# Optimization experiments

Measured on AMD Instinct MI355X. Metric: run time of the kernel, lower is better.

## Reference

```python
import jax, jax.numpy as jnp
import numpy as np

N = 50000      # nodes
E = 800000     # edges (before self loops)
DIN = 128      # input_dim
H = 128        # hidden_dim
DOUT = 64      # output_dim
G = 64         # graphs in batch
EATTR = 16     # edge_attr dim (unused by math, kept for signature fidelity)


def _conv_params(key, din, h, scale=0.05):
    ks = jax.random.split(key, 6)
    return dict(
        lin_w=jax.random.normal(ks[0], (din, h), dtype=jnp.float32) * scale,
        lin_b=jnp.zeros((h,), jnp.float32),
        w1=jax.random.normal(ks[1], (2 * h, h), dtype=jnp.float32) * scale,
        b1=jnp.zeros((h,), jnp.float32),
        w2=jax.random.normal(ks[2], (h, h), dtype=jnp.float32) * scale,
        b2=jnp.zeros((h,), jnp.float32),
    )


def setup_inputs() -> dict:
    key = jax.random.key(0)
    ks = jax.random.split(key, 10)
    inp = {
        'x': jax.random.normal(ks[0], (N, DIN), dtype=jnp.float32),
        'edge_index': jax.random.randint(ks[1], (2, E), 0, N),
        'edge_attr': jax.random.normal(ks[2], (E, EATTR), dtype=jnp.float32),
        'batch': jnp.sort(jax.random.randint(ks[3], (N,), 0, G)),
    }
    p1 = _conv_params(ks[4], DIN, H)
    p2 = _conv_params(ks[5], H, H)
    p3 = _conv_params(ks[6], H, H)
    for i, p in enumerate((p1, p2, p3), start=1):
        for k, v in p.items():
            inp[f'c{i}_{k}'] = v
    inp['out_w'] = jax.random.normal(ks[7], (H, DOUT), dtype=jnp.float32) * 0.05
    inp['out_b'] = jnp.zeros((DOUT,), jnp.float32)
    return inp


def mpnn_conv(x, src, dst, lin_w, lin_b, w1, b1, w2, b2):
    # x: [N, din] -> h: [N, H]
    n = x.shape[0]
    h = x @ lin_w + lin_b
    loop = jnp.arange(n)
    s = jnp.concatenate([src, loop])   # x_j (source) indices, self loops appended
    d = jnp.concatenate([dst, loop])   # x_i (target) indices
    z = jnp.concatenate([h[d], h[s]], axis=-1)          # [E+N, 2H]  (cat[x_i, x_j])
    m = jax.nn.relu(z @ w1 + b1) @ w2 + b2              # [E+N, H]
    return jax.ops.segment_sum(m, d, num_segments=n)    # aggr='add' at targets


def reference(x, edge_index, edge_attr, batch,
              c1_lin_w, c1_lin_b, c1_w1, c1_b1, c1_w2, c1_b2,
              c2_lin_w, c2_lin_b, c2_w1, c2_b1, c2_w2, c2_b2,
              c3_lin_w, c3_lin_b, c3_w1, c3_b1, c3_w2, c3_b2,
              out_w, out_b):
    src, dst = edge_index[0], edge_index[1]
    h = jax.nn.relu(mpnn_conv(x, src, dst, c1_lin_w, c1_lin_b, c1_w1, c1_b1, c1_w2, c1_b2))
    h = jax.nn.relu(mpnn_conv(h, src, dst, c2_lin_w, c2_lin_b, c2_w1, c2_b1, c2_w2, c2_b2))
    h = jax.nn.relu(mpnn_conv(h, src, dst, c3_lin_w, c3_lin_b, c3_w1, c3_b1, c3_w2, c3_b2))
    # global_mean_pool over graphs
    sums = jax.ops.segment_sum(h, batch, num_segments=G)                       # [G, H]
    cnts = jax.ops.segment_sum(jnp.ones((h.shape[0],), h.dtype), batch, num_segments=G)
    pooled = sums / jnp.maximum(cnts, 1.0)[:, None]
    return pooled @ out_w + out_b
```

## Files before the change

### kernel.cpp

```cpp
#include <hip/hip_runtime.h>
#include <hip/hip_bf16.h>


typedef _Float16 f16_t;
typedef f16_t f16x2 __attribute__((ext_vector_type(2)));
typedef f16_t f16x8 __attribute__((ext_vector_type(8)));
typedef float f32x4 __attribute__((ext_vector_type(4)));
typedef float f32x2v __attribute__((ext_vector_type(2)));
typedef unsigned int u32;
typedef unsigned short u16;
typedef unsigned char u8;

__device__ __forceinline__ float f16lo(u32 v) {
    return (float)__builtin_bit_cast(f16_t, (u16)(v & 0xffff));
}
__device__ __forceinline__ float f16hi(u32 v) {
    return (float)__builtin_bit_cast(f16_t, (u16)(v >> 16));
}
__device__ __forceinline__ u16 f16b(float x) { return __builtin_bit_cast(u16, (f16_t)x); }
__device__ __forceinline__ u32 f16pack(float x, float y) {
    return (u32)f16b(x) | ((u32)f16b(y) << 16);
}

typedef __attribute__((address_space(1))) void gvoid_t;
typedef __attribute__((address_space(3))) void lvoid_t;
__device__ __forceinline__ void glds16(const void* g, void* l) {
    __builtin_amdgcn_global_load_lds((gvoid_t*)g, (lvoid_t*)l, 16, 0, 0);
}

struct PrepArgs {
    const float* x; f16_t* xb; int totalx;
    const int* ei; int E;
    int* hist; int nbk; int NB;
    const float* lin_w[3]; const float* lin_b[3];
    const float* w1[3]; const float* b1[3]; const float* w2[3];
    f16_t* linw16;
    f16_t* w1T;
    f16_t* W2t;
    float* bias256c;
};

__global__ __launch_bounds__(256) void prep_kernel(PrepArgs A, int nConvB) {
    __shared__ union { int hist[512]; u16 T16[128 * 130]; } shm;
    const int b = blockIdx.x, tid = threadIdx.x;
    const int nTr = 9, nLw = 48, nBias = 3;
    if (b < nTr) {
        int layer = b / 3, which = b % 3;
        const float* src; f16_t* dst;
        if (which == 0)      { src = A.w1[layer];          dst = A.w1T + layer * 32768; }
        else if (which == 1) { src = A.w1[layer] + 16384;  dst = A.w1T + layer * 32768 + 16384; }
        else                 { src = A.w2[layer];          dst = A.W2t + layer * 16384; }
#pragma unroll
        for (int it = 0; it < 16; ++it) {
            int idx = it * 1024 + tid * 4;
            int r = idx >> 7, c = idx & 127;
            float4 v = *(const float4*)(src + idx);
            *(u32*)&shm.T16[r * 130 + c] = f16pack(v.x, v.y);
            *(u32*)&shm.T16[r * 130 + c + 2] = f16pack(v.z, v.w);
        }
        __syncthreads();
#pragma unroll
        for (int it = 0; it < 32; ++it) {
            int o = it * 256 + tid;
            int j = o >> 6, c = (o & 63) * 2;
            u32 w = (u32)shm.T16[c * 130 + j] | ((u32)shm.T16[(c + 1) * 130 + j] << 16);
            ((u32*)dst)[o] = w;
        }
        return;
    }
    if (b < nTr + nLw) {
        int i = (b - nTr) * 1024 + tid * 4;
        int layer = i >> 14, off = i & 16383;
        float4 v = *(const float4*)(A.lin_w[layer] + off);
        *(uint2*)(A.linw16 + i) = make_uint2(f16pack(v.x, v.y), f16pack(v.z, v.w));
        return;
    }
    if (b < nTr + nLw + nBias) {
        int layer = b - nTr - nLw;
        int j = tid;
        const float* w1p = A.w1[layer];
        const float* wcol = (j < 128) ? (w1p + j) : (w1p + 16384 + (j - 128));
        const float* lbp = A.lin_b[layer];
        float s = (j < 128) ? A.b1[layer][j] : 0.f;
        for (int c = 0; c < 128; ++c) s += lbp[c] * wcol[c * 128];
        A.bias256c[layer * 256 + j] = s;
        return;
    }
    if (b < nTr + nLw + nBias + A.NB) {
        const int bb = b - nTr - nLw - nBias;
        const int nbk = A.nbk, E = A.E;
        for (int i = tid; i < nbk; i += 256) shm.hist[i] = 0;
        __syncthreads();
        const int chunk = (E + A.NB - 1) / A.NB;
        const int e0 = bb * chunk, e1 = min(E, e0 + chunk);
        for (int e = e0 + tid; e < e1; e += 256) atomicAdd(&shm.hist[A.ei[E + e] >> 7], 1);
        __syncthreads();
        for (int i = tid; i < nbk; i += 256) A.hist[(size_t)bb * nbk + i] = shm.hist[i];
        return;
    }
    int i = ((b - nTr - nLw - nBias - A.NB) * 256 + tid) * 4;
    if (i >= A.totalx) return;
    float4 v = *(const float4*)(A.x + i);
    *(uint2*)(A.xb + i) = make_uint2(f16pack(v.x, v.y), f16pack(v.z, v.w));
}

__global__ __launch_bounds__(256) void hscan_kernel(int* __restrict__ hist,
                                                    int* __restrict__ bcnt, int nbk, int NB) {
    __shared__ int sh[256];
    const int b = blockIdx.x, t = threadIdx.x;
    int run = 0;
    for (int c0 = 0; c0 < NB; c0 += 256) {
        int idx = c0 + t;
        int v = (idx < NB) ? hist[(size_t)idx * nbk + b] : 0;
        sh[t] = v;
        __syncthreads();
#pragma unroll
        for (int o = 1; o < 256; o <<= 1) {
            int u = (t >= o) ? sh[t - o] : 0;
            __syncthreads();
            sh[t] += u;
            __syncthreads();
        }
        if (idx < NB) hist[(size_t)idx * nbk + b] = run + sh[t] - v;
        int tot = sh[255];
        __syncthreads();
        run += tot;
    }
    if (t == 0) bcnt[b] = run;
}

__global__ __launch_bounds__(256) void scat_kernel(const int* __restrict__ ei,
                                                   const int* __restrict__ hist,
                                                   u32* __restrict__ bbuf, int E, int NB,
                                                   int nbk, int cap) {
    __shared__ int basep[512];
    __shared__ int cnt2[512];
    const int bb = blockIdx.x, t = threadIdx.x;
    for (int i = t; i < nbk; i += 256) {
        basep[i] = hist[(size_t)bb * nbk + i];
        cnt2[i] = 0;
    }
    __syncthreads();
    const int chunk = (E + NB - 1) / NB;
    const int e0 = bb * chunk, e1 = min(E, e0 + chunk);
    for (int e = e0 + t; e < e1; e += 256) {
        int dst = ei[E + e], src = ei[e];
        int bkt = dst >> 7;
        int r = atomicAdd(&cnt2[bkt], 1);
        int pp = basep[bkt] + r;
        if (pp < cap) bbuf[(size_t)bkt * cap + pp] = ((u32)(dst & 127) << 16) | (u32)src;
    }
}

__global__ __launch_bounds__(128) void part2_kernel(const u32* __restrict__ bbuf,
                                                    const int* __restrict__ bcnt,
                                                    int* __restrict__ row_ptr,
                                                    float* __restrict__ cntp1f,
                                                    int* __restrict__ bsumB, int cap, int N) {
    __shared__ int ldeg[128];
    __shared__ int sh[128];
    const int b = blockIdx.x, t = threadIdx.x;
    ldeg[t] = 0;
    __syncthreads();
    const int cnt = min(bcnt[b], cap);
    const u32* p = bbuf + (size_t)b * cap;
    for (int i = t; i < cnt; i += 128) atomicAdd(&ldeg[p[i] >> 16], 1);
    __syncthreads();
    int d = ldeg[t];
    sh[t] = d;
    __syncthreads();
#pragma unroll
    for (int o = 1; o < 128; o <<= 1) {
        int u = (t >= o) ? sh[t - o] : 0;
        __syncthreads();
        sh[t] += u;
        __syncthreads();
    }
    int node = (b << 7) + t;
    if (node < N) {
        row_ptr[node] = sh[t] - d;
        cntp1f[node] = (float)(d + 1);
    }
    if (t == 127) bsumB[b] = sh[127];
}

__global__ __launch_bounds__(512) void scanb_kernel(const int* __restrict__ bsumB,
                                                    int* __restrict__ bbase,
                                                    int* __restrict__ row_ptr, int nbk, int N) {
    __shared__ int sh[512];
    const int t = threadIdx.x;
    int v = (t < nbk) ? bsumB[t] : 0;
    sh[t] = v;
    __syncthreads();
#pragma unroll
    for (int o = 1; o < 512; o <<= 1) {
        int u = (t >= o) ? sh[t - o] : 0;
        __syncthreads();
        sh[t] += u;
        __syncthreads();
    }
    if (t < nbk) bbase[t] = sh[t] - v;
    if (t == 511) row_ptr[N] = sh[511];
}

__global__ __launch_bounds__(128) void part3_kernel(const u32* __restrict__ bbuf,
                                                    const int* __restrict__ bcnt,
                                                    const int* __restrict__ bbase,
                                                    int* __restrict__ row_ptr,
                                                    u16* __restrict__ colarr, int cap, int N) {
    __shared__ int lcur[128];
    const int b = blockIdx.x, t = threadIdx.x;
    const int node = (b << 7) + t;
    const int bb = bbase[b];
    int rp = 0;
    if (node < N) {
        rp = row_ptr[node] + bb;
        row_ptr[node] = rp;
    }
    lcur[t] = rp;
    __syncthreads();
    const int cnt = min(bcnt[b], cap);
    const u32* p = bbuf + (size_t)b * cap;
    for (int i = t; i < cnt; i += 128) {
        u32 en = p[i];
        int addr = atomicAdd(&lcur[en >> 16], 1);
        colarr[addr] = (u16)(en & 0xffffu);
    }
}

__device__ __forceinline__ void gemm_tile(const f16_t* __restrict__ X,
                                          const f16_t* __restrict__ Wt,
                                          const float* __restrict__ bias,
                                          const float* __restrict__ bias2,
                                          const float* __restrict__ rowscale,
                                          f16_t* __restrict__ Y, u8* __restrict__ Y8, int N,
                                          int ldc, int relu_flag, int row0, int coloff) {
    __shared__ f16_t sX[128 * 128];
    __shared__ f16_t sW[128 * 128];
    const int tid = threadIdx.x;
    const int wave = tid >> 6, lane = tid & 63;
#pragma unroll
    for (int it = 0; it < 8; ++it) {
        int idx = it * 256 + tid;
        int r = idx >> 4, c8 = idx & 15;
        int gr = row0 + r;
        if (gr >= N) gr = 0;
        glds16(X + (size_t)gr * 128 + ((c8 ^ (r & 7)) * 8),
               sX + (size_t)(it * 256 + (wave << 6)) * 8);
    }
#pragma unroll
    for (int it = 0; it < 8; ++it) {
        int idx = it * 256 + tid;
        int r = idx >> 4, c8 = idx & 15;
        glds16(Wt + (size_t)(coloff + r) * 128 + ((c8 ^ (r & 7)) * 8),
               sW + (size_t)(it * 256 + (wave << 6)) * 8);
    }
    __syncthreads();
    const int m = lane & 15, q = lane >> 4;
    const int sw = m & 7;
    f32x4 acc[2][8];
#pragma unroll
    for (int rt = 0; rt < 2; ++rt)
#pragma unroll
        for (int t = 0; t < 8; ++t) acc[rt][t] = (f32x4){0.f, 0.f, 0.f, 0.f};
#pragma unroll
    for (int kk = 0; kk < 4; ++kk) {
        const int g = (kk * 4 + q) ^ sw;
        f16x8 a0 = *(const f16x8*)(&sX[(wave * 32 + m) * 128 + g * 8]);
        f16x8 a1 = *(const f16x8*)(&sX[(wave * 32 + 16 + m) * 128 + g * 8]);
#pragma unroll
        for (int t = 0; t < 8; ++t) {
            f16x8 bfr = *(const f16x8*)(&sW[(t * 16 + m) * 128 + g * 8]);
            acc[0][t] = __builtin_amdgcn_mfma_f32_16x16x32_f16(a0, bfr, acc[0][t], 0, 0, 0);
            acc[1][t] = __builtin_amdgcn_mfma_f32_16x16x32_f16(a1, bfr, acc[1][t], 0, 0, 0);
        }
    }
#pragma unroll
    for (int t = 0; t < 8; ++t) {
        int col = coloff + t * 16 + m;
        float bv = bias ? bias[col] : 0.f;
        float b2v = bias2 ? bias2[col] : 0.f;
#pragma unroll
        for (int rt = 0; rt < 2; ++rt) {
#pragma unroll
            for (int j = 0; j < 4; ++j) {
                int rl = wave * 32 + rt * 16 + q * 4 + j;
                int gr = row0 + rl;
                float v = acc[rt][t][j] + bv;
                if (rowscale && gr < N) v += rowscale[gr] * b2v;
                if (relu_flag) v = fmaxf(v, 0.f);
                sX[rl * 128 + ((t * 16 + m) ^ ((rl & 4) << 3))] = (f16_t)v;
            }
        }
    }
    const bool fp8p = (Y8 != nullptr) && (coloff == 128);
    if (!fp8p) {
#pragma unroll
        for (int it = 0; it < 8; ++it) {
            int i64 = it * 64 + lane;
            int rl = (wave << 5) + (i64 >> 4), c8 = i64 & 15;
            int gr = row0 + rl;
            uint4 v = *(const uint4*)(&sX[rl * 128 + ((c8 ^ (rl & 4)) * 8)]);
            if (gr < N) *(uint4*)(Y + (size_t)gr * ldc + coloff + c8 * 8) = v;
        }
    } else {
#pragma unroll
        for (int it = 0; it < 8; ++it) {
            int i64 = it * 64 + lane;
            int rl = (wave << 5) + (i64 >> 4), c8 = i64 & 15;
            int gr = row0 + rl;
            const u32* p = (const u32*)&sX[rl * 128 + ((c8 ^ (rl & 4)) * 8)];
            u32 lo = __builtin_amdgcn_cvt_pk_fp8_f32(f16lo(p[0]), f16hi(p[0]), 0u, false);
            lo = __builtin_amdgcn_cvt_pk_fp8_f32(f16lo(p[1]), f16hi(p[1]), lo, true);
            u32 hi = __builtin_amdgcn_cvt_pk_fp8_f32(f16lo(p[2]), f16hi(p[2]), 0u, false);
            hi = __builtin_amdgcn_cvt_pk_fp8_f32(f16lo(p[3]), f16hi(p[3]), hi, true);
            if (gr < N) *(uint2*)(Y8 + (size_t)gr * 128 + c8 * 8) = make_uint2(lo, hi);
        }
    }
}

__global__ __launch_bounds__(256) void gemm_node(const f16_t* __restrict__ X,
                                                 const f16_t* __restrict__ Wt,
                                                 const float* __restrict__ bias,
                                                 const float* __restrict__ bias2,
                                                 const float* __restrict__ rowscale,
                                                 f16_t* __restrict__ Y, u8* __restrict__ Y8,
                                                 int N, int ldc, int relu_flag) {
    gemm_tile(X, Wt, bias, bias2, rowscale, Y, Y8, N, ldc, relu_flag, blockIdx.x * 128,
              blockIdx.y * 128);
}

__global__ __launch_bounds__(256) void compose_kernel(const f16_t* __restrict__ w1T,
                                                      const f16_t* __restrict__ linw16,
                                                      f16_t* __restrict__ W12ct) {
    int layer = blockIdx.x >> 1, rb = blockIdx.x & 1;
    gemm_tile(w1T + layer * 32768, linw16 + layer * 16384, nullptr, nullptr, nullptr,
              W12ct + layer * 32768, nullptr, 256, 128, 0, rb * 128, 0);
}

__global__ __launch_bounds__(256) void gather_kernel(const f16_t* __restrict__ aArr,
                                                     const u8* __restrict__ b8,
                                                     const int* __restrict__ row_ptr,
                                                     const u16* __restrict__ colarr,
                                                     f16_t* __restrict__ q, int N) {
    int wid = (blockIdx.x * 256 + threadIdx.x) >> 6;
    int lane = threadIdx.x & 63;
    if (wid >= N) return;
    const int g = lane >> 4, l = lane & 15;
    uint4 A = ((const uint4*)aArr)[(size_t)wid * 16 + l];
    float a0 = f16lo(A.x), a1 = f16hi(A.x), a2 = f16lo(A.y), a3 = f16hi(A.y);
    float a4 = f16lo(A.z), a5 = f16hi(A.z), a6 = f16lo(A.w), a7 = f16hi(A.w);
    float c0 = 0.f, c1 = 0.f, c2 = 0.f, c3 = 0.f, c4 = 0.f, c5 = 0.f, c6 = 0.f, c7 = 0.f;
    const uint2* b8u = (const uint2*)b8;
    auto accum = [&](uint2 B) {
        f32x2v p0 = __builtin_amdgcn_cvt_pk_f32_fp8(B.x, false);
        f32x2v p1 = __builtin_amdgcn_cvt_pk_f32_fp8(B.x, true);
        f32x2v p2 = __builtin_amdgcn_cvt_pk_f32_fp8(B.y, false);
        f32x2v p3 = __builtin_amdgcn_cvt_pk_f32_fp8(B.y, true);
        c0 += fmaxf(a0 + p0.x, 0.f); c1 += fmaxf(a1 + p0.y, 0.f);
        c2 += fmaxf(a2 + p1.x, 0.f); c3 += fmaxf(a3 + p1.y, 0.f);
        c4 += fmaxf(a4 + p2.x, 0.f); c5 += fmaxf(a5 + p2.y, 0.f);
        c6 += fmaxf(a6 + p3.x, 0.f); c7 += fmaxf(a7 + p3.y, 0.f);
    };
    if (g == 0) accum(b8u[(size_t)wid * 16 + l]);
    int e0 = row_ptr[wid], e1 = row_ptr[wid + 1];
    int e = e0;
    for (; e + 16 <= e1; e += 16) {
        int s0 = colarr[e + g], s1 = colarr[e + 4 + g];
        int s2 = colarr[e + 8 + g], s3 = colarr[e + 12 + g];
        uint2 B0 = b8u[(size_t)s0 * 16 + l];
        uint2 B1 = b8u[(size_t)s1 * 16 + l];
        uint2 B2 = b8u[(size_t)s2 * 16 + l];
        uint2 B3 = b8u[(size_t)s3 * 16 + l];
        accum(B0); accum(B1); accum(B2); accum(B3);
    }
    for (; e < e1; e += 4) {
        int i0 = e + g;
        if (i0 < e1) accum(b8u[(size_t)colarr[i0] * 16 + l]);
    }
#pragma unroll
    for (int off = 16; off < 64; off <<= 1) {
        c0 += __shfl_xor(c0, off); c1 += __shfl_xor(c1, off);
        c2 += __shfl_xor(c2, off); c3 += __shfl_xor(c3, off);
        c4 += __shfl_xor(c4, off); c5 += __shfl_xor(c5, off);
        c6 += __shfl_xor(c6, off); c7 += __shfl_xor(c7, off);
    }
    if (g == 0) {
        uint4 o;
        o.x = f16pack(c0, c1); o.y = f16pack(c2, c3);
        o.z = f16pack(c4, c5); o.w = f16pack(c6, c7);
        ((uint4*)q)[(size_t)wid * 16 + l] = o;
    }
}

__global__ __launch_bounds__(256) void pool_kernel(const f16_t* __restrict__ agg,
                                                   const int* __restrict__ batch,
                                                   float* __restrict__ pooled,
                                                   int* __restrict__ cntg, int N) {
    int wid = (blockIdx.x * 256 + threadIdx.x) >> 6;
    int lane = threadIdx.x & 63;
    int n0 = wid * 32;
    if (n0 >= N) return;
    int n1 = min(n0 + 32, N);
    const u32* au = (const u32*)agg;
    int gcur = batch[n0];
    float sx = 0.f, sy = 0.f;
    int cnt = 0;
    for (int n = n0; n < n1; ++n) {
        int g = batch[n];
        if (g != gcur) {
            atomicAdd(&pooled[gcur * 128 + lane * 2], sx);
            atomicAdd(&pooled[gcur * 128 + lane * 2 + 1], sy);
            if (lane == 0) atomicAdd(&cntg[gcur], cnt);
            gcur = g; sx = 0.f; sy = 0.f; cnt = 0;
        }
        u32 v = au[(size_t)n * 64 + lane];
        sx += f16lo(v);
        sy += f16hi(v);
        ++cnt;
    }
    atomicAdd(&pooled[gcur * 128 + lane * 2], sx);
    atomicAdd(&pooled[gcur * 128 + lane * 2 + 1], sy);
    if (lane == 0) atomicAdd(&cntg[gcur], cnt);
}

__global__ __launch_bounds__(256) void final_kernel(const float* __restrict__ pooled,
                                                    const int* __restrict__ cntg,
                                                    const float* __restrict__ out_w,
                                                    const float* __restrict__ out_b,
                                                    float* __restrict__ out, int total) {
    int idx = blockIdx.x * 256 + threadIdx.x;
    if (idx >= total) return;
    int g = idx >> 6, o = idx & 63;
    float c = fmaxf((float)cntg[g], 1.0f);
    float s = 0.f;
#pragma unroll 4
    for (int k = 0; k < 128; ++k) s += pooled[g * 128 + k] * out_w[k * 64 + o];
    out[idx] = s / c + out_b[o];
}

extern "C" void kernel_launch(void* const* d_in, const int* in_sizes, int n_in, void* d_out,
                              int out_size, void* d_ws, size_t ws_size, hipStream_t stream) {
    const float* x = (const float*)d_in[0];
    const int* ei = (const int*)d_in[1];
    const int* batch = (const int*)d_in[3];
    const float* cw[3][6];
    for (int l = 0; l < 3; ++l)
        for (int j = 0; j < 6; ++j) cw[l][j] = (const float*)d_in[4 + l * 6 + j];
    const float* out_w = (const float*)d_in[22];
    const float* out_b = (const float*)d_in[23];
    float* out = (float*)d_out;

    const int N = in_sizes[0] / 128;
    const int E = in_sizes[1] / 2;
    const int G = out_size / 64;
    const int nbk = (N + 127) >> 7;
    const int NB = 416;
    const int cap = E / nbk + 512;

    char* base = (char*)d_ws;
    size_t off = 0;
    auto alloc = [&](size_t b) { size_t o = off; off += (b + 255) & ~(size_t)255; return o; };
    float* pooled = (float*)(base + alloc((size_t)G * 128 * 4));
    int* cntg = (int*)(base + alloc((size_t)G * 4));
    const size_t zero_bytes = off;
    int* hist = (int*)(base + alloc((size_t)NB * nbk * 4));
    int* bcnt = (int*)(base + alloc((size_t)nbk * 4));
    int* bsumB = (int*)(base + alloc((size_t)nbk * 4));
    int* bbase = (int*)(base + alloc((size_t)nbk * 4));
    int* row_ptr = (int*)(base + alloc((size_t)(N + 1) * 4));
    float* cntp1f = (float*)(base + alloc((size_t)N * 4));
    u16* colarr = (u16*)(base + alloc((size_t)E * 2));
    u32* bbuf = (u32*)(base + alloc((size_t)nbk * cap * 4));
    f16_t* xb = (f16_t*)(base + alloc((size_t)N * 128 * 2));
    f16_t* q = (f16_t*)(base + alloc((size_t)N * 128 * 2));
    f16_t* aArr = (f16_t*)(base + alloc((size_t)N * 128 * 2));
    u8* b8 = (u8*)(base + alloc((size_t)N * 128));
    f16_t* linw16 = (f16_t*)(base + alloc(3 * 16384 * 2));
    f16_t* w1T = (f16_t*)(base + alloc(3 * 32768 * 2));
    f16_t* W12ct = (f16_t*)(base + alloc(3 * 32768 * 2));
    f16_t* W2t = (f16_t*)(base + alloc(3 * 16384 * 2));
    float* bias256c = (float*)(base + alloc(3 * 256 * 4));
    (void)ws_size; (void)n_in;

    hipMemsetAsync(d_ws, 0, zero_bytes, stream);

    PrepArgs pa;
    pa.x = x; pa.xb = xb; pa.totalx = N * 128;
    pa.ei = ei; pa.E = E;
    pa.hist = hist; pa.nbk = nbk; pa.NB = NB;
    for (int l = 0; l < 3; ++l) {
        pa.lin_w[l] = cw[l][0]; pa.lin_b[l] = cw[l][1];
        pa.w1[l] = cw[l][2]; pa.b1[l] = cw[l][3]; pa.w2[l] = cw[l][4];
    }
    pa.linw16 = linw16; pa.w1T = w1T; pa.W2t = W2t; pa.bias256c = bias256c;
    const int nConvB = (N * 128 / 4 + 255) / 256;
    prep_kernel<<<9 + 48 + 3 + NB + nConvB, 256, 0, stream>>>(pa, nConvB);

    compose_kernel<<<6, 256, 0, stream>>>(w1T, linw16, W12ct);

    hscan_kernel<<<nbk, 256, 0, stream>>>(hist, bcnt, nbk, NB);
    scat_kernel<<<NB, 256, 0, stream>>>(ei, hist, bbuf, E, NB, nbk, cap);
    part2_kernel<<<nbk, 128, 0, stream>>>(bbuf, bcnt, row_ptr, cntp1f, bsumB, cap, N);
    scanb_kernel<<<1, 512, 0, stream>>>(bsumB, bbase, row_ptr, nbk, N);
    part3_kernel<<<nbk, 128, 0, stream>>>(bbuf, bcnt, bbase, row_ptr, colarr, cap, N);

    const int gblocks = (N + 127) / 128;
    const f16_t* Xin = xb;
    for (int l = 0; l < 3; ++l) {
        gemm_node<<<dim3(gblocks, 2), 256, 0, stream>>>(Xin, W12ct + l * 32768,
                                                        bias256c + l * 256, nullptr, nullptr,
                                                        aArr, b8, N, 128, 0);
        gather_kernel<<<(N * 64 + 255) / 256, 256, 0, stream>>>(aArr, b8, row_ptr, colarr, q, N);
        gemm_node<<<dim3(gblocks, 1), 256, 0, stream>>>(q, W2t + l * 16384, nullptr, cw[l][5],
                                                        cntp1f, xb, nullptr, N, 128, 1);
        Xin = xb;
    }

    pool_kernel<<<((N + 31) / 32 * 64 + 255) / 256, 256, 0, stream>>>(Xin, batch, pooled, cntg, N);
    final_kernel<<<(G * 64 + 255) / 256, 256, 0, stream>>>(pooled, cntg, out_w, out_b, out,
                                                           G * 64);
}
```

Measured before the change: 409.2 us.

## Replace per-tile node GEMMs with persistent double-buffered kernels keeping weights resident

The node GEMMs are now launched as persistent 512-thread blocks on a grid of at most 256. Each block loads the full weight matrix (both 128-column halves for the first GEMM) into shared memory once, then loops over row tiles with double-buffered X loads, so the next tile's load overlaps the current MFMA work. The 2D grid that split the output columns across blocks goes away, which removes repeated X and W loads. The cost is more LDS per block (one block per CU) and extra syncs, and the epilogue stages each wave's results through a per-wave 16-row region of the current X buffer.

```diff
diff --git a/kernel.cpp b/kernel.cpp
--- a/kernel.cpp
+++ b/kernel.cpp
@@ -230,11 +230,8 @@
 
 __device__ __forceinline__ void gemm_tile(const f16_t* __restrict__ X,
                                           const f16_t* __restrict__ Wt,
-                                          const float* __restrict__ bias,
-                                          const float* __restrict__ bias2,
-                                          const float* __restrict__ rowscale,
-                                          f16_t* __restrict__ Y, u8* __restrict__ Y8, int N,
-                                          int ldc, int relu_flag, int row0, int coloff) {
+                                          f16_t* __restrict__ Y, int N,
+                                          int ldc, int row0) {
     __shared__ f16_t sX[128 * 128];
     __shared__ f16_t sW[128 * 128];
     const int tid = threadIdx.x;
@@ -252,7 +249,7 @@
     for (int it = 0; it < 8; ++it) {
         int idx = it * 256 + tid;
         int r = idx >> 4, c8 = idx & 15;
-        glds16(Wt + (size_t)(coloff + r) * 128 + ((c8 ^ (r & 7)) * 8),
+        glds16(Wt + (size_t)r * 128 + ((c8 ^ (r & 7)) * 8),
                sW + (size_t)(it * 256 + (wave << 6)) * 8);
     }
     __syncthreads();
@@ -277,65 +274,151 @@
     }
 #pragma unroll
     for (int t = 0; t < 8; ++t) {
-        int col = coloff + t * 16 + m;
-        float bv = bias ? bias[col] : 0.f;
-        float b2v = bias2 ? bias2[col] : 0.f;
+        int col = t * 16 + m;
 #pragma unroll
         for (int rt = 0; rt < 2; ++rt) {
 #pragma unroll
             for (int j = 0; j < 4; ++j) {
-                int rl = wave * 32 + rt * 16 + q * 4 + j;
-                int gr = row0 + rl;
-                float v = acc[rt][t][j] + bv;
-                if (rowscale && gr < N) v += rowscale[gr] * b2v;
-                if (relu_flag) v = fmaxf(v, 0.f);
-                sX[rl * 128 + ((t * 16 + m) ^ ((rl & 4) << 3))] = (f16_t)v;
+                int r = row0 + wave * 32 + rt * 16 + q * 4 + j;
+                if (r < N) Y[(size_t)r * ldc + col] = (f16_t)acc[rt][t][j];
             }
         }
     }
-    const bool fp8p = (Y8 != nullptr) && (coloff == 128);
-    if (!fp8p) {
-#pragma unroll
-        for (int it = 0; it < 8; ++it) {
-            int i64 = it * 64 + lane;
-            int rl = (wave << 5) + (i64 >> 4), c8 = i64 & 15;
-            int gr = row0 + rl;
-            uint4 v = *(const uint4*)(&sX[rl * 128 + ((c8 ^ (rl & 4)) * 8)]);
-            if (gr < N) *(uint4*)(Y + (size_t)gr * ldc + coloff + c8 * 8) = v;
-        }
-    } else {
-#pragma unroll
-        for (int it = 0; it < 8; ++it) {
-            int i64 = it * 64 + lane;
-            int rl = (wave << 5) + (i64 >> 4), c8 = i64 & 15;
-            int gr = row0 + rl;
-            const u32* p = (const u32*)&sX[rl * 128 + ((c8 ^ (rl & 4)) * 8)];
-            u32 lo = __builtin_amdgcn_cvt_pk_fp8_f32(f16lo(p[0]), f16hi(p[0]), 0u, false);
-            lo = __builtin_amdgcn_cvt_pk_fp8_f32(f16lo(p[1]), f16hi(p[1]), lo, true);
-            u32 hi = __builtin_amdgcn_cvt_pk_fp8_f32(f16lo(p[2]), f16hi(p[2]), 0u, false);
-            hi = __builtin_amdgcn_cvt_pk_fp8_f32(f16lo(p[3]), f16hi(p[3]), hi, true);
-            if (gr < N) *(uint2*)(Y8 + (size_t)gr * 128 + c8 * 8) = make_uint2(lo, hi);
-        }
-    }
-}
-
-__global__ __launch_bounds__(256) void gemm_node(const f16_t* __restrict__ X,
-                                                 const f16_t* __restrict__ Wt,
-                                                 const float* __restrict__ bias,
-                                                 const float* __restrict__ bias2,
-                                                 const float* __restrict__ rowscale,
-                                                 f16_t* __restrict__ Y, u8* __restrict__ Y8,
-                                                 int N, int ldc, int relu_flag) {
-    gemm_tile(X, Wt, bias, bias2, rowscale, Y, Y8, N, ldc, relu_flag, blockIdx.x * 128,
-              blockIdx.y * 128);
 }
 
 __global__ __launch_bounds__(256) void compose_kernel(const f16_t* __restrict__ w1T,
                                                       const f16_t* __restrict__ linw16,
                                                       f16_t* __restrict__ W12ct) {
     int layer = blockIdx.x >> 1, rb = blockIdx.x & 1;
-    gemm_tile(w1T + layer * 32768, linw16 + layer * 16384, nullptr, nullptr, nullptr,
-              W12ct + layer * 32768, nullptr, 256, 128, 0, rb * 128, 0);
+    gemm_tile(w1T + layer * 32768, linw16 + layer * 16384, W12ct + layer * 32768, 256, 128,
+              rb * 128);
+}
+
+template <int NT>
+__global__ __launch_bounds__(512, 1) void gemm_persist(
+    const f16_t* __restrict__ X, const f16_t* __restrict__ Wt,
+    const float* __restrict__ bias, const float* __restrict__ bias2,
+    const float* __restrict__ rowscale, f16_t* __restrict__ Y, u8* __restrict__ Y8,
+    int N, int relu_flag, int ntiles) {
+    __shared__ f16_t sW[NT * 16 * 128];
+    __shared__ f16_t sX[2][128 * 128];
+    const int tid = threadIdx.x;
+    const int wave = tid >> 6, lane = tid & 63;
+    const int m = lane & 15, q = lane >> 4, sw = m & 7;
+    constexpr int NR = (NT == 16) ? 2 : 1;
+    const int rb0 = (NT == 16) ? ((wave & 3) * 32) : (wave * 16);
+    const int chalf = (NT == 16) ? (wave >> 2) : 0;
+
+#pragma unroll
+    for (int it = 0; it < NT / 2; ++it) {
+        int idx = it * 512 + tid;
+        int r = idx >> 4, c8 = idx & 15;
+        glds16(Wt + (size_t)r * 128 + ((c8 ^ (r & 7)) * 8),
+               sW + (size_t)(it * 512 + (wave << 6)) * 8);
+    }
+    float bvv[8], b2vv[8];
+#pragma unroll
+    for (int t2 = 0; t2 < 8; ++t2) {
+        int colb = chalf * 128 + t2 * 16 + m;
+        bvv[t2] = bias ? bias[colb] : 0.f;
+        b2vv[t2] = bias2 ? bias2[colb] : 0.f;
+    }
+    int t = blockIdx.x;
+    {
+        int row0 = t * 128;
+#pragma unroll
+        for (int it = 0; it < 4; ++it) {
+            int idx = it * 512 + tid;
+            int r = idx >> 4, c8 = idx & 15;
+            int gr = row0 + r;
+            if (gr >= N) gr = 0;
+            glds16(X + (size_t)gr * 128 + ((c8 ^ (r & 7)) * 8),
+                   sX[0] + (size_t)(it * 512 + (wave << 6)) * 8);
+        }
+    }
+    __syncthreads();
+    int cur = 0;
+    for (; t < ntiles; t += gridDim.x) {
+        const int row0 = t * 128;
+        const int tn = t + gridDim.x;
+        f16_t* sXc = sX[cur];
+        if (tn < ntiles) {
+            const int r0n = tn * 128;
+            f16_t* sXn = sX[cur ^ 1];
+#pragma unroll
+            for (int it = 0; it < 4; ++it) {
+                int idx = it * 512 + tid;
+                int r = idx >> 4, c8 = idx & 15;
+                int gr = r0n + r;
+                if (gr >= N) gr = 0;
+                glds16(X + (size_t)gr * 128 + ((c8 ^ (r & 7)) * 8),
+                       sXn + (size_t)(it * 512 + (wave << 6)) * 8);
+            }
+        }
+        f32x4 acc[NR][8];
+#pragma unroll
+        for (int rt = 0; rt < NR; ++rt)
+#pragma unroll
+            for (int t2 = 0; t2 < 8; ++t2) acc[rt][t2] = (f32x4){0.f, 0.f, 0.f, 0.f};
+#pragma unroll
+        for (int kk = 0; kk < 4; ++kk) {
+            const int g = (kk * 4 + q) ^ sw;
+            f16x8 a0 = *(const f16x8*)(&sXc[(rb0 + m) * 128 + g * 8]);
+            f16x8 a1{};
+            if constexpr (NR == 2) a1 = *(const f16x8*)(&sXc[(rb0 + 16 + m) * 128 + g * 8]);
+#pragma unroll
+            for (int t2 = 0; t2 < 8; ++t2) {
+                f16x8 bfr =
+                    *(const f16x8*)(&sW[(size_t)(chalf * 128 + t2 * 16 + m) * 128 + g * 8]);
+                acc[0][t2] = __builtin_amdgcn_mfma_f32_16x16x32_f16(a0, bfr, acc[0][t2], 0, 0, 0);
+                if constexpr (NR == 2)
+                    acc[1][t2] =
+                        __builtin_amdgcn_mfma_f32_16x16x32_f16(a1, bfr, acc[1][t2], 0, 0, 0);
+            }
+        }
+        if (NT == 16) __syncthreads();
+        f16_t* region = sXc + wave * 16 * 128;
+#pragma unroll
+        for (int rt = 0; rt < NR; ++rt) {
+            float rs[4];
+#pragma unroll
+            for (int j = 0; j < 4; ++j) {
+                int gr = row0 + rb0 + rt * 16 + q * 4 + j;
+                rs[j] = (bias2 && gr < N) ? rowscale[gr] : 0.f;
+            }
+#pragma unroll
+            for (int t2 = 0; t2 < 8; ++t2) {
+#pragma unroll
+                for (int j = 0; j < 4; ++j) {
+                    int rl2 = q * 4 + j;
+                    float v = acc[rt][t2][j] + bvv[t2];
+                    if (bias2) v += rs[j] * b2vv[t2];
+                    if (relu_flag) v = fmaxf(v, 0.f);
+                    region[rl2 * 128 + ((t2 * 16 + m) ^ ((rl2 & 4) << 3))] = (f16_t)v;
+                }
+            }
+#pragma unroll
+            for (int it2 = 0; it2 < 4; ++it2) {
+                int i = it2 * 64 + lane;
+                int rl = i >> 4, c8 = i & 15;
+                int gr = row0 + rb0 + rt * 16 + rl;
+                const f16_t* rp = &region[rl * 128 + ((c8 ^ (rl & 4)) * 8)];
+                if (NT == 16 && chalf == 1) {
+                    const u32* p = (const u32*)rp;
+                    u32 lo = __builtin_amdgcn_cvt_pk_fp8_f32(f16lo(p[0]), f16hi(p[0]), 0u, false);
+                    lo = __builtin_amdgcn_cvt_pk_fp8_f32(f16lo(p[1]), f16hi(p[1]), lo, true);
+                    u32 hi = __builtin_amdgcn_cvt_pk_fp8_f32(f16lo(p[2]), f16hi(p[2]), 0u, false);
+                    hi = __builtin_amdgcn_cvt_pk_fp8_f32(f16lo(p[3]), f16hi(p[3]), hi, true);
+                    if (gr < N) *(uint2*)(Y8 + (size_t)gr * 128 + c8 * 8) = make_uint2(lo, hi);
+                } else {
+                    uint4 v4 = *(const uint4*)rp;
+                    if (gr < N) *(uint4*)(Y + (size_t)gr * 128 + c8 * 8) = v4;
+                }
+            }
+        }
+        __syncthreads();
+        cur ^= 1;
+    }
 }
 
 __global__ __launch_bounds__(256) void gather_kernel(const f16_t* __restrict__ aArr,
@@ -505,15 +588,16 @@
     scanb_kernel<<<1, 512, 0, stream>>>(bsumB, bbase, row_ptr, nbk, N);
     part3_kernel<<<nbk, 128, 0, stream>>>(bbuf, bcnt, bbase, row_ptr, colarr, cap, N);
 
-    const int gblocks = (N + 127) / 128;
+    const int ntiles = (N + 127) >> 7;
+    const int pgrid = (ntiles < 256) ? ntiles : 256;
     const f16_t* Xin = xb;
     for (int l = 0; l < 3; ++l) {
-        gemm_node<<<dim3(gblocks, 2), 256, 0, stream>>>(Xin, W12ct + l * 32768,
-                                                        bias256c + l * 256, nullptr, nullptr,
-                                                        aArr, b8, N, 128, 0);
+        gemm_persist<16><<<pgrid, 512, 0, stream>>>(Xin, W12ct + l * 32768,
+                                                    bias256c + l * 256, nullptr, nullptr,
+                                                    aArr, b8, N, 0, ntiles);
         gather_kernel<<<(N * 64 + 255) / 256, 256, 0, stream>>>(aArr, b8, row_ptr, colarr, q, N);
-        gemm_node<<<dim3(gblocks, 1), 256, 0, stream>>>(q, W2t + l * 16384, nullptr, cw[l][5],
-                                                        cntp1f, xb, nullptr, N, 128, 1);
+        gemm_persist<8><<<pgrid, 512, 0, stream>>>(q, W2t + l * 16384, nullptr, cw[l][5],
+                                                   cntp1f, xb, nullptr, N, 1, ntiles);
         Xin = xb;
     }
 
```

Result: faster. 387.8 us (-5.2%).
